# Kernel optimization log

Hardware: AMD Instinct MI355X
Metric: run time of the kernel (lower is better)

Reference implementation:

```python
import jax, jax.numpy as jnp
import numpy as np

# Hyperparameters (from init_kwargs)
N = 100000      # num_nodes
T = 4           # num_edge_type
E = 400000      # edges per type
C = 2           # num_channels
L = 2           # num_layers
W_IN = 128      # input feature dim
D = 64          # node_dim (w_out)
NUM_CLASS = 16
BETA = 0.5
M = 10000       # number of target nodes


def setup_inputs() -> dict:
    key = jax.random.key(0)
    ks = jax.random.split(key, 10)
    glorot = np.sqrt(6.0 / (W_IN + D))
    glorot1 = np.sqrt(6.0 / (C * D + D))
    glorot2 = np.sqrt(6.0 / (D + NUM_CLASS))
    return {
        "X": jax.random.normal(ks[0], (N, W_IN), dtype=jnp.float32),
        "edge_value": jax.random.uniform(ks[1], (T, E), dtype=jnp.float32),
        "conv_weights": 0.1 * jax.random.normal(ks[2], (L, C, T), dtype=jnp.float32),
        "Ws": jax.random.uniform(ks[3], (C, W_IN, D), minval=-glorot, maxval=glorot, dtype=jnp.float32),
        "lin1_w": jax.random.uniform(ks[4], (C * D, D), minval=-glorot1, maxval=glorot1, dtype=jnp.float32),
        "lin1_b": jnp.zeros((D,), dtype=jnp.float32),
        "lin_w": jax.random.uniform(ks[5], (D, NUM_CLASS), minval=-glorot2, maxval=glorot2, dtype=jnp.float32),
        "lin_b": jnp.zeros((NUM_CLASS,), dtype=jnp.float32),
        "edge_index": jax.random.randint(ks[6], (T, 2, E), 0, N),
        "target_x": jax.random.randint(ks[7], (M,), 0, N),
    }


def reference(X, edge_value, conv_weights, Ws, lin1_w, lin1_b, lin_w, lin_b,
              edge_index, target_x):
    # Flatten edge types into one big edge list. torch_sparse.coalesce(op='add')
    # followed by torch.sparse.mm is mathematically a duplicate-summing SpMM,
    # i.e. a segment_sum over destination rows.
    rows = edge_index[:, 0, :].reshape(-1)      # [T*E]
    cols = edge_index[:, 1, :].reshape(-1)      # [T*E]
    vals = edge_value.reshape(-1)               # [T*E]
    type_id = jnp.repeat(jnp.arange(T), E)      # [T*E] edge-type id (constant)

    # Per-channel input projections: X_ = X @ Ws[c]  -> [C, N, D]
    X_ = jnp.einsum('nf,cfd->cnd', X, Ws)
    H = X_

    for l in range(L):
        # FastGTConv: softmax over edge types per channel
        filt = jax.nn.softmax(conv_weights[l], axis=1)   # [C, T]
        newH = []
        for c in range(C):
            v = vals * filt[c, type_id]                  # [T*E] mixed edge weights
            msgs = v[:, None] * H[c][cols]               # gather + scale: [T*E, D]
            newH.append(jax.ops.segment_sum(msgs, rows, num_segments=N))
        H = jnp.stack(newH)                              # [C, N, D]

    # FastGTN tail: relu(beta*X_ + (1-beta)*H), concat channels, linear1
    Hc = jax.nn.relu(BETA * X_ + (1.0 - BETA) * H)       # [C, N, D]
    Hcat = jnp.transpose(Hc, (1, 0, 2)).reshape(N, C * D)
    H_ = Hcat @ lin1_w + lin1_b                          # [N, D]

    # FastGTNs head: logits at target nodes
    return H_[target_x] @ lin_w + lin_b                  # [M, NUM_CLASS]
```

## Files before the change

kernel.cpp:

```cpp
#include <hip/hip_runtime.h>

#define N_NODES   100000
#define T_TYPES   4
#define E_EDGES   400000
#define E4        100000
#define G_TOT     400000
#define TE_TOT    1600000
#define C_CH      2
#define L_LAYERS  2
#define W_INF     128
#define DD        64
#define NUM_CLASS 16
#define BETA      0.5f
#define M_TGT     10000

#define NBKT      196
#define BROWS     512
#define BPAD      9216
#define CHUNK_G   512
#define NPART_BLK ((G_TOT + CHUNK_G - 1) / CHUNK_G)

static const size_t PLANE2 = (size_t)N_NODES * DD;

typedef __attribute__((ext_vector_type(8))) short short8x;
typedef __attribute__((ext_vector_type(4))) float f32x4;

__device__ __forceinline__ unsigned bf16rne(float x) {
    unsigned u = __float_as_uint(x);
    return (u + 0x7FFFu + ((u >> 16) & 1u)) >> 16;
}
__device__ __forceinline__ unsigned packbf(float a, float b) {
    return bf16rne(a) | (bf16rne(b) << 16);
}
__device__ __forceinline__ float bflo(unsigned u) { return __uint_as_float(u << 16); }
__device__ __forceinline__ float bfhi(unsigned u) { return __uint_as_float(u & 0xFFFF0000u); }

__device__ __forceinline__ void load_filter(const float* cw, int layer,
                                            float* f0, float* f1) {
    float m0 = -1e30f, m1 = -1e30f;
    #pragma unroll
    for (int t = 0; t < T_TYPES; ++t) {
        f0[t] = cw[layer * C_CH * T_TYPES + t];
        f1[t] = cw[layer * C_CH * T_TYPES + T_TYPES + t];
        m0 = fmaxf(m0, f0[t]); m1 = fmaxf(m1, f1[t]);
    }
    float s0 = 0.f, s1 = 0.f;
    #pragma unroll
    for (int t = 0; t < T_TYPES; ++t) {
        f0[t] = __expf(f0[t] - m0); s0 += f0[t];
        f1[t] = __expf(f1[t] - m1); s1 += f1[t];
    }
    #pragma unroll
    for (int t = 0; t < T_TYPES; ++t) { f0[t] /= s0; f1[t] /= s1; }
}

__global__ void prep_kernel(const float* __restrict__ Ws,
                            unsigned short* __restrict__ Wsb,
                            int* __restrict__ cursor) {
    int b = blockIdx.x;
    int tid = threadIdx.x;
    if (b < 64) {
        int idx = b * 256 + tid;
        int c   = idx >> 13;
        int rem = idx & 8191;
        int d   = rem >> 7;
        int k   = rem & 127;
        Wsb[idx] = (unsigned short)bf16rne(Ws[c * (W_INF * DD) + k * DD + d]);
    } else {
        if (tid < NBKT) cursor[tid] = tid * BPAD;
    }
}

#define AROW 136
__global__ __launch_bounds__(256) void proj_mfma(const float* __restrict__ X,
                                                 const unsigned short* __restrict__ Wsb,
                                                 unsigned* __restrict__ Xp16) {
    __shared__ unsigned short a_lds[64 * AROW];
    int tid  = threadIdx.x;
    int row0 = blockIdx.x * 64;

    const float4* X4 = (const float4*)X;
    #pragma unroll
    for (int i = 0; i < 8; ++i) {
        int gi = tid + 256 * i;
        int r  = gi >> 5;
        int c4 = gi & 31;
        int row = row0 + r;
        float4 v = make_float4(0.f, 0.f, 0.f, 0.f);
        if (row < N_NODES) v = X4[(size_t)row * 32 + c4];
        *(uint2*)&a_lds[r * AROW + c4 * 4] = make_uint2(packbf(v.x, v.y),
                                                        packbf(v.z, v.w));
    }
    __syncthreads();

    int wave = tid >> 6, lane = tid & 63;
    int m = lane & 15, q = lane >> 4;

    short8x A[4];
    #pragma unroll
    for (int ks = 0; ks < 4; ++ks)
        A[ks] = *(const short8x*)&a_lds[(wave * 16 + m) * AROW + ks * 32 + q * 8];

    #pragma unroll
    for (int ct = 0; ct < 4; ++ct) {
        f32x4 acc0 = {0.f, 0.f, 0.f, 0.f};
        f32x4 acc1 = {0.f, 0.f, 0.f, 0.f};
        #pragma unroll
        for (int ks = 0; ks < 4; ++ks) {
            short8x B0 = *(const short8x*)(Wsb + (ct * 16 + m) * 128 + ks * 32 + q * 8);
            short8x B1 = *(const short8x*)(Wsb + 8192 + (ct * 16 + m) * 128 + ks * 32 + q * 8);
            acc0 = __builtin_amdgcn_mfma_f32_16x16x32_bf16(A[ks], B0, acc0, 0, 0, 0);
            acc1 = __builtin_amdgcn_mfma_f32_16x16x32_bf16(A[ks], B1, acc1, 0, 0, 0);
        }
        #pragma unroll
        for (int r = 0; r < 4; ++r) {
            int row = row0 + wave * 16 + q * 4 + r;
            if (row < N_NODES)
                Xp16[(size_t)row * DD + ct * 16 + m] = packbf(acc0[r], acc1[r]);
        }
    }
}

__global__ __launch_bounds__(256) void partition_kernel(const int* __restrict__ edge_index,
                                                        const float* __restrict__ edge_value,
                                                        const float* __restrict__ cw,
                                                        int* __restrict__ cursor,
                                                        int2* __restrict__ edata2) {
    __shared__ int cnt[NBKT];
    __shared__ int lbase[NBKT];
    __shared__ int gbase[NBKT];
    __shared__ int2 le[CHUNK_G * 4];
    __shared__ unsigned char lbk[CHUNK_G * 4];
    int tid = threadIdx.x;
    if (tid < NBKT) cnt[tid] = 0;
    __syncthreads();

    float f0[T_TYPES], f1[T_TYPES];
    load_filter(cw, 0, f0, f1);

    int px[8], pv[8], rk[8], bk[8];
    int ne = 0;
    #pragma unroll
    for (int g = 0; g < 2; ++g) {
        int idx = blockIdx.x * CHUNK_G + g * 256 + tid;
        if (idx < G_TOT) {
            int t = idx / E4, r = idx - t * E4;
            const int* bptr = edge_index + (size_t)t * 2 * E_EDGES;
            int4   rw = ((const int4*)bptr)[r];
            int4   cl = ((const int4*)(bptr + E_EDGES))[r];
            float4 vv = ((const float4*)(edge_value + (size_t)t * E_EDGES))[r];
            int tb = t << 17;
            int   rr[4] = {rw.x, rw.y, rw.z, rw.w};
            int   cc[4] = {cl.x, cl.y, cl.z, cl.w};
            float vf[4] = {vv.x, vv.y, vv.z, vv.w};
            #pragma unroll
            for (int k = 0; k < 4; ++k) {
                int b = rr[k] >> 9;
                px[ne] = cc[k] | tb | ((rr[k] & 511) << 19);
                pv[ne] = __float_as_int(vf[k]);
                bk[ne] = b;
                rk[ne] = atomicAdd(&cnt[b], 1);
                ++ne;
            }
        }
    }
    __syncthreads();
    if (tid < 64) {
        int c[4]; int s = 0;
        #pragma unroll
        for (int k = 0; k < 4; ++k) {
            int idx = tid * 4 + k;
            c[k] = (idx < NBKT) ? cnt[idx] : 0;
            s += c[k];
        }
        int inc = s;
        #pragma unroll
        for (int off = 1; off < 64; off <<= 1) {
            int v = __shfl_up(inc, off);
            if (tid >= off) inc += v;
        }
        int base = inc - s;
        #pragma unroll
        for (int k = 0; k < 4; ++k) {
            int idx = tid * 4 + k;
            if (idx < NBKT) lbase[idx] = base;
            base += c[k];
        }
    }
    __syncthreads();
    #pragma unroll
    for (int k = 0; k < 8; ++k) {
        if (k < ne) {
            int slot = lbase[bk[k]] + rk[k];
            le[slot]  = make_int2(px[k], pv[k]);
            lbk[slot] = (unsigned char)bk[k];
        }
    }
    __syncthreads();
    if (tid < NBKT) gbase[tid] = cnt[tid] ? atomicAdd(&cursor[tid], cnt[tid]) : 0;
    __syncthreads();
    int ngrp = min(CHUNK_G, G_TOT - blockIdx.x * CHUNK_G);
    int nloc = 4 * ngrp;
    for (int j = tid; j < nloc; j += 256) {
        int b = lbk[j];
        int2 e = le[j];
        int t = (e.x >> 17) & 3;
        float v = __int_as_float(e.y);
        edata2[gbase[b] + (j - lbase[b])] =
            make_int2(e.x, (int)packbf(v * f0[t], v * f1[t]));
    }
}

__global__ __launch_bounds__(1024) void rowsort_kernel(const int* __restrict__ cursor,
                                                       int2* __restrict__ edata2,
                                                       int* __restrict__ offs) {
    __shared__ int rcnt[BROWS];
    __shared__ int rbase[BROWS];
    __shared__ int rcur[BROWS];
    __shared__ int2 le[BPAD];
    int b   = blockIdx.x;
    int tid = threadIdx.x;
    int bb  = b * BPAD;
    int cnt = cursor[b] - bb;
    if (tid < BROWS) rcnt[tid] = 0;
    __syncthreads();
    for (int j = tid; j < cnt; j += 1024) {
        int2 e = edata2[bb + j];
        le[j] = e;
        atomicAdd(&rcnt[(e.x >> 19) & 511], 1);
    }
    __syncthreads();
    if (tid < 64) {
        int c[8]; int s = 0;
        #pragma unroll
        for (int k = 0; k < 8; ++k) { c[k] = rcnt[tid * 8 + k]; s += c[k]; }
        int inc = s;
        #pragma unroll
        for (int off = 1; off < 64; off <<= 1) {
            int v = __shfl_up(inc, off);
            if (tid >= off) inc += v;
        }
        int base = inc - s;
        #pragma unroll
        for (int k = 0; k < 8; ++k) { rbase[tid * 8 + k] = base; base += c[k]; }
    }
    __syncthreads();
    if (tid < BROWS) rcur[tid] = rbase[tid];
    __syncthreads();
    for (int j = tid; j < cnt; j += 1024) {
        int2 e = le[j];
        int lr = (e.x >> 19) & 511;
        int pos = atomicAdd(&rcur[lr], 1);
        edata2[bb + pos] = e;
    }
    int row0  = b * BROWS;
    int nrows = min(BROWS, N_NODES - row0);
    if (tid < nrows)
        offs[row0 + tid] = bb + rbase[tid] + rcnt[tid];
}

__device__ __forceinline__ void edge_fma(const uint2 h, unsigned wp, float4& acc) {
    float w0 = bflo(wp), w1 = bfhi(wp);
    acc.x = fmaf(w0, bflo(h.x), acc.x);
    acc.y = fmaf(w1, bfhi(h.x), acc.y);
    acc.z = fmaf(w0, bflo(h.y), acc.z);
    acc.w = fmaf(w1, bfhi(h.y), acc.w);
}

__device__ __forceinline__ int row_beg(const int* offs, int row) {
    return ((row & 511) == 0) ? (row >> 9) * BPAD : offs[row - 1];
}

__global__ __launch_bounds__(256) void spmm_gather(const uint2* __restrict__ Hin16,
                                                   uint2* __restrict__ Hout16,
                                                   const int* __restrict__ offs,
                                                   const int2* __restrict__ edata2) {
    int lane = threadIdx.x & 63;
    int slot = lane & 31, sub = lane >> 5;
    int row  = (blockIdx.x * blockDim.x + threadIdx.x) >> 6;
    int beg = row_beg(offs, row);
    int end = offs[row];
    float4 acc = make_float4(0.f, 0.f, 0.f, 0.f);
    int i = beg + sub;
    for (; i + 6 < end; i += 8) {
        int2 e0 = edata2[i];
        int2 e1 = edata2[i + 2];
        int2 e2 = edata2[i + 4];
        int2 e3 = edata2[i + 6];
        uint2 h0 = Hin16[(size_t)((e0.x & 0x1FFFF) * 32 + slot)];
        uint2 h1 = Hin16[(size_t)((e1.x & 0x1FFFF) * 32 + slot)];
        uint2 h2 = Hin16[(size_t)((e2.x & 0x1FFFF) * 32 + slot)];
        uint2 h3 = Hin16[(size_t)((e3.x & 0x1FFFF) * 32 + slot)];
        edge_fma(h0, (unsigned)e0.y, acc);
        edge_fma(h1, (unsigned)e1.y, acc);
        edge_fma(h2, (unsigned)e2.y, acc);
        edge_fma(h3, (unsigned)e3.y, acc);
    }
    for (; i < end; i += 2) {
        int2 e = edata2[i];
        uint2 h = Hin16[(size_t)((e.x & 0x1FFFF) * 32 + slot)];
        edge_fma(h, (unsigned)e.y, acc);
    }
    acc.x += __shfl_xor(acc.x, 32);
    acc.y += __shfl_xor(acc.y, 32);
    acc.z += __shfl_xor(acc.z, 32);
    acc.w += __shfl_xor(acc.w, 32);
    if (sub == 0)
        Hout16[(size_t)row * 32 + slot] = make_uint2(packbf(acc.x, acc.y),
                                                     packbf(acc.z, acc.w));
}

__global__ __launch_bounds__(256) void tgt_tail_kernel(const uint2* __restrict__ Hin16,
                                                       const unsigned* __restrict__ Xp16,
                                                       const int* __restrict__ offs,
                                                       const int2* __restrict__ edata2,
                                                       const float* __restrict__ cw,
                                                       const int* __restrict__ tgt,
                                                       const float* __restrict__ lin1_w,
                                                       const float* __restrict__ lin1_b,
                                                       const float* __restrict__ lin_w,
                                                       const float* __restrict__ lin_b,
                                                       float* __restrict__ out) {
    __shared__ float l1w[W_INF * DD];
    __shared__ float lw[DD * NUM_CLASS];
    __shared__ float l1b[DD];
    __shared__ float lb[NUM_CLASS];
    __shared__ float hc[4][W_INF];
    __shared__ float hmid[4][DD];

    int tid = threadIdx.x;
    {
        const float4* g = (const float4*)lin1_w;
        float4* s = (float4*)l1w;
        #pragma unroll
        for (int i = 0; i < 8; ++i) s[tid + 256 * i] = g[tid + 256 * i];
        ((float4*)lw)[tid] = ((const float4*)lin_w)[tid];
        if (tid < DD) l1b[tid] = lin1_b[tid];
        else if (tid < DD + NUM_CLASS) lb[tid - DD] = lin_b[tid - DD];
    }

    float f0a[T_TYPES], f1a[T_TYPES], f0b[T_TYPES], f1b[T_TYPES];
    load_filter(cw, 0, f0a, f1a);
    load_filter(cw, 1, f0b, f1b);
    float r0[T_TYPES], r1[T_TYPES];
    #pragma unroll
    for (int t = 0; t < T_TYPES; ++t) { r0[t] = f0b[t] / f0a[t]; r1[t] = f1b[t] / f1a[t]; }

    int w = tid >> 6, lane = tid & 63;
    int slot = lane & 31, sub = lane >> 5;
    int m = blockIdx.x * 4 + w;
    int row = tgt[m];
    int beg = row_beg(offs, row);
    int end = offs[row];
    float4 acc = make_float4(0.f, 0.f, 0.f, 0.f);
    for (int i = beg + sub; i < end; i += 2) {
        int2 e = edata2[i];
        int t = (e.x >> 17) & 3;
        uint2 h = Hin16[(size_t)((e.x & 0x1FFFF) * 32 + slot)];
        unsigned wp = (unsigned)e.y;
        float w0 = bflo(wp) * r0[t], w1 = bfhi(wp) * r1[t];
        acc.x = fmaf(w0, bflo(h.x), acc.x);
        acc.y = fmaf(w1, bfhi(h.x), acc.y);
        acc.z = fmaf(w0, bflo(h.y), acc.z);
        acc.w = fmaf(w1, bfhi(h.y), acc.w);
    }
    acc.x += __shfl_xor(acc.x, 32);
    acc.y += __shfl_xor(acc.y, 32);
    acc.z += __shfl_xor(acc.z, 32);
    acc.w += __shfl_xor(acc.w, 32);

    if (sub == 0) {
        uint2 xu = ((const uint2*)Xp16)[(size_t)row * 32 + slot];
        int d0 = 2 * slot, d1 = 2 * slot + 1;
        hc[w][d0]      = fmaxf(BETA * bflo(xu.x) + (1.f - BETA) * acc.x, 0.f);
        hc[w][DD + d0] = fmaxf(BETA * bfhi(xu.x) + (1.f - BETA) * acc.y, 0.f);
        hc[w][d1]      = fmaxf(BETA * bflo(xu.y) + (1.f - BETA) * acc.z, 0.f);
        hc[w][DD + d1] = fmaxf(BETA * bfhi(xu.y) + (1.f - BETA) * acc.w, 0.f);
    }
    __syncthreads();

    float a1 = l1b[lane];
    #pragma unroll 8
    for (int k = 0; k < W_INF; ++k)
        a1 = fmaf(hc[w][k], l1w[k * DD + lane], a1);
    hmid[w][lane] = a1;
    __syncthreads();

    if (lane < NUM_CLASS) {
        float o = lb[lane];
        #pragma unroll 8
        for (int k = 0; k < DD; ++k)
            o = fmaf(hmid[w][k], lw[k * NUM_CLASS + lane], o);
        out[(size_t)m * NUM_CLASS + lane] = o;
    }
}

extern "C" void kernel_launch(void* const* d_in, const int* in_sizes, int n_in,
                              void* d_out, int out_size, void* d_ws, size_t ws_size,
                              hipStream_t stream) {
    const float* X            = (const float*)d_in[0];
    const float* edge_value   = (const float*)d_in[1];
    const float* conv_weights = (const float*)d_in[2];
    const float* Ws           = (const float*)d_in[3];
    const float* lin1_w       = (const float*)d_in[4];
    const float* lin1_b       = (const float*)d_in[5];
    const float* lin_w        = (const float*)d_in[6];
    const float* lin_b        = (const float*)d_in[7];
    const int*   edge_index   = (const int*)d_in[8];
    const int*   target_x     = (const int*)d_in[9];
    float* out = (float*)d_out;

    unsigned*       Xp16 = (unsigned*)d_ws;
    unsigned*       H116 = Xp16 + PLANE2;
    unsigned short* Wsb  = (unsigned short*)(H116 + PLANE2);
    int*            offs = (int*)(Wsb + C_CH * W_INF * DD);
    int*            cursor = offs + N_NODES;
    int2*           edata2 = (int2*)(cursor + 256);

    prep_kernel<<<65, 256, 0, stream>>>(Ws, Wsb, cursor);
    partition_kernel<<<NPART_BLK, 256, 0, stream>>>(edge_index, edge_value,
                                                    conv_weights, cursor, edata2);
    proj_mfma<<<(N_NODES + 63) / 64, 256, 0, stream>>>(X, Wsb, Xp16);
    rowsort_kernel<<<NBKT, 1024, 0, stream>>>(cursor, edata2, offs);
    spmm_gather<<<(N_NODES * 64) / 256, 256, 0, stream>>>((const uint2*)Xp16,
                                                          (uint2*)H116, offs, edata2);
    tgt_tail_kernel<<<M_TGT / 4, 256, 0, stream>>>((const uint2*)H116, Xp16, offs,
                                                   edata2, conv_weights, target_x,
                                                   lin1_w, lin1_b, lin_w, lin_b, out);
}
```

Before: 273.5 us.

## Fuse partition with projection, shrink row buckets, widen gather loads to 16 bytes

Merges the edge-partition and MFMA projection kernels into one launch, with blocks picking their role from the block index, so the two independent phases can run together. Bucket size drops from 512 to 256 rows: more buckets, smaller padding, and a rowsort with 512 threads. The SpMM gather and target tail now load 16-byte uint4 chunks, with four edges in flight per wave and a two-step shuffle reduction. The risks are more shared memory per block in the fused kernel and less memory-level parallelism per lane in the gather.

```diff
diff --git a/kernel.cpp b/kernel.cpp
--- a/kernel.cpp
+++ b/kernel.cpp
@@ -14,11 +14,12 @@
 #define BETA      0.5f
 #define M_TGT     10000
 
-#define NBKT      196
-#define BROWS     512
-#define BPAD      9216
-#define CHUNK_G   512
-#define NPART_BLK ((G_TOT + CHUNK_G - 1) / CHUNK_G)
+#define NBKT      391
+#define BROWS     256
+#define BPAD      4864
+#define CHUNK_G   1024
+#define NPART_BLK 391
+#define PROJ_BLK  1563
 
 static const size_t PLANE2 = (size_t)N_NODES * DD;
 
@@ -67,153 +68,162 @@
         int k   = rem & 127;
         Wsb[idx] = (unsigned short)bf16rne(Ws[c * (W_INF * DD) + k * DD + d]);
     } else {
-        if (tid < NBKT) cursor[tid] = tid * BPAD;
+        int idx = (b - 64) * 256 + tid;
+        if (idx < NBKT) cursor[idx] = idx * BPAD;
     }
 }
 
 #define AROW 136
-__global__ __launch_bounds__(256) void proj_mfma(const float* __restrict__ X,
-                                                 const unsigned short* __restrict__ Wsb,
-                                                 unsigned* __restrict__ Xp16) {
-    __shared__ unsigned short a_lds[64 * AROW];
-    int tid  = threadIdx.x;
-    int row0 = blockIdx.x * 64;
-
-    const float4* X4 = (const float4*)X;
-    #pragma unroll
-    for (int i = 0; i < 8; ++i) {
-        int gi = tid + 256 * i;
-        int r  = gi >> 5;
-        int c4 = gi & 31;
-        int row = row0 + r;
-        float4 v = make_float4(0.f, 0.f, 0.f, 0.f);
-        if (row < N_NODES) v = X4[(size_t)row * 32 + c4];
-        *(uint2*)&a_lds[r * AROW + c4 * 4] = make_uint2(packbf(v.x, v.y),
-                                                        packbf(v.z, v.w));
-    }
-    __syncthreads();
-
-    int wave = tid >> 6, lane = tid & 63;
-    int m = lane & 15, q = lane >> 4;
-
-    short8x A[4];
-    #pragma unroll
-    for (int ks = 0; ks < 4; ++ks)
-        A[ks] = *(const short8x*)&a_lds[(wave * 16 + m) * AROW + ks * 32 + q * 8];
-
-    #pragma unroll
-    for (int ct = 0; ct < 4; ++ct) {
-        f32x4 acc0 = {0.f, 0.f, 0.f, 0.f};
-        f32x4 acc1 = {0.f, 0.f, 0.f, 0.f};
-        #pragma unroll
-        for (int ks = 0; ks < 4; ++ks) {
-            short8x B0 = *(const short8x*)(Wsb + (ct * 16 + m) * 128 + ks * 32 + q * 8);
-            short8x B1 = *(const short8x*)(Wsb + 8192 + (ct * 16 + m) * 128 + ks * 32 + q * 8);
-            acc0 = __builtin_amdgcn_mfma_f32_16x16x32_bf16(A[ks], B0, acc0, 0, 0, 0);
-            acc1 = __builtin_amdgcn_mfma_f32_16x16x32_bf16(A[ks], B1, acc1, 0, 0, 0);
-        }
-        #pragma unroll
-        for (int r = 0; r < 4; ++r) {
-            int row = row0 + wave * 16 + q * 4 + r;
-            if (row < N_NODES)
-                Xp16[(size_t)row * DD + ct * 16 + m] = packbf(acc0[r], acc1[r]);
-        }
-    }
-}
-
-__global__ __launch_bounds__(256) void partition_kernel(const int* __restrict__ edge_index,
-                                                        const float* __restrict__ edge_value,
-                                                        const float* __restrict__ cw,
-                                                        int* __restrict__ cursor,
-                                                        int2* __restrict__ edata2) {
-    __shared__ int cnt[NBKT];
-    __shared__ int lbase[NBKT];
-    __shared__ int gbase[NBKT];
-    __shared__ int2 le[CHUNK_G * 4];
-    __shared__ unsigned char lbk[CHUNK_G * 4];
+#define SMEM_BYTES 45664
+
+__global__ __launch_bounds__(256) void build_proj_kernel(
+        const int* __restrict__ edge_index,
+        const float* __restrict__ edge_value,
+        const float* __restrict__ cw,
+        int* __restrict__ cursor,
+        int2* __restrict__ edata2,
+        const float* __restrict__ X,
+        const unsigned short* __restrict__ Wsb,
+        unsigned* __restrict__ Xp16) {
+    __shared__ __align__(16) char smem[SMEM_BYTES];
     int tid = threadIdx.x;
-    if (tid < NBKT) cnt[tid] = 0;
-    __syncthreads();
-
-    float f0[T_TYPES], f1[T_TYPES];
-    load_filter(cw, 0, f0, f1);
-
-    int px[8], pv[8], rk[8], bk[8];
-    int ne = 0;
-    #pragma unroll
-    for (int g = 0; g < 2; ++g) {
-        int idx = blockIdx.x * CHUNK_G + g * 256 + tid;
-        if (idx < G_TOT) {
-            int t = idx / E4, r = idx - t * E4;
-            const int* bptr = edge_index + (size_t)t * 2 * E_EDGES;
-            int4   rw = ((const int4*)bptr)[r];
-            int4   cl = ((const int4*)(bptr + E_EDGES))[r];
-            float4 vv = ((const float4*)(edge_value + (size_t)t * E_EDGES))[r];
-            int tb = t << 17;
-            int   rr[4] = {rw.x, rw.y, rw.z, rw.w};
-            int   cc[4] = {cl.x, cl.y, cl.z, cl.w};
-            float vf[4] = {vv.x, vv.y, vv.z, vv.w};
+
+    if (blockIdx.x < NPART_BLK) {
+        int* cnt   = (int*)smem;
+        int* lbase = cnt + 392;
+        int* gbase = lbase + 392;
+        int2* le   = (int2*)(smem + 4704);
+        unsigned short* lbk = (unsigned short*)(smem + 4704 + 32768);
+
+        int p = blockIdx.x;
+        for (int j = tid; j < NBKT; j += 256) cnt[j] = 0;
+        __syncthreads();
+
+        float f0[T_TYPES], f1[T_TYPES];
+        load_filter(cw, 0, f0, f1);
+
+        int px[16], pv[16], rk[16], bk[16];
+        int ne = 0;
+        #pragma unroll
+        for (int g = 0; g < 4; ++g) {
+            int idx = p * CHUNK_G + g * 256 + tid;
+            if (idx < G_TOT) {
+                int t = idx / E4, r = idx - t * E4;
+                const int* bptr = edge_index + (size_t)t * 2 * E_EDGES;
+                int4   rw = ((const int4*)bptr)[r];
+                int4   cl = ((const int4*)(bptr + E_EDGES))[r];
+                float4 vv = ((const float4*)(edge_value + (size_t)t * E_EDGES))[r];
+                int tb = t << 17;
+                int   rr[4] = {rw.x, rw.y, rw.z, rw.w};
+                int   cc[4] = {cl.x, cl.y, cl.z, cl.w};
+                float vf[4] = {vv.x, vv.y, vv.z, vv.w};
+                #pragma unroll
+                for (int k = 0; k < 4; ++k) {
+                    int b = rr[k] >> 8;
+                    px[ne] = cc[k] | tb | ((rr[k] & 255) << 19);
+                    pv[ne] = __float_as_int(vf[k]);
+                    bk[ne] = b;
+                    rk[ne] = atomicAdd(&cnt[b], 1);
+                    ++ne;
+                }
+            }
+        }
+        __syncthreads();
+        if (tid < 64) {
+            int c[7]; int s = 0;
             #pragma unroll
-            for (int k = 0; k < 4; ++k) {
-                int b = rr[k] >> 9;
-                px[ne] = cc[k] | tb | ((rr[k] & 511) << 19);
-                pv[ne] = __float_as_int(vf[k]);
-                bk[ne] = b;
-                rk[ne] = atomicAdd(&cnt[b], 1);
-                ++ne;
-            }
-        }
-    }
-    __syncthreads();
-    if (tid < 64) {
-        int c[4]; int s = 0;
-        #pragma unroll
-        for (int k = 0; k < 4; ++k) {
-            int idx = tid * 4 + k;
-            c[k] = (idx < NBKT) ? cnt[idx] : 0;
-            s += c[k];
-        }
-        int inc = s;
-        #pragma unroll
-        for (int off = 1; off < 64; off <<= 1) {
-            int v = __shfl_up(inc, off);
-            if (tid >= off) inc += v;
-        }
-        int base = inc - s;
-        #pragma unroll
-        for (int k = 0; k < 4; ++k) {
-            int idx = tid * 4 + k;
-            if (idx < NBKT) lbase[idx] = base;
-            base += c[k];
-        }
-    }
-    __syncthreads();
-    #pragma unroll
-    for (int k = 0; k < 8; ++k) {
-        if (k < ne) {
-            int slot = lbase[bk[k]] + rk[k];
-            le[slot]  = make_int2(px[k], pv[k]);
-            lbk[slot] = (unsigned char)bk[k];
-        }
-    }
-    __syncthreads();
-    if (tid < NBKT) gbase[tid] = cnt[tid] ? atomicAdd(&cursor[tid], cnt[tid]) : 0;
-    __syncthreads();
-    int ngrp = min(CHUNK_G, G_TOT - blockIdx.x * CHUNK_G);
-    int nloc = 4 * ngrp;
-    for (int j = tid; j < nloc; j += 256) {
-        int b = lbk[j];
-        int2 e = le[j];
-        int t = (e.x >> 17) & 3;
-        float v = __int_as_float(e.y);
-        edata2[gbase[b] + (j - lbase[b])] =
-            make_int2(e.x, (int)packbf(v * f0[t], v * f1[t]));
-    }
-}
-
-__global__ __launch_bounds__(1024) void rowsort_kernel(const int* __restrict__ cursor,
-                                                       int2* __restrict__ edata2,
-                                                       int* __restrict__ offs) {
+            for (int k = 0; k < 7; ++k) {
+                int idx = tid * 7 + k;
+                c[k] = (idx < NBKT) ? cnt[idx] : 0;
+                s += c[k];
+            }
+            int inc = s;
+            #pragma unroll
+            for (int off = 1; off < 64; off <<= 1) {
+                int v = __shfl_up(inc, off);
+                if (tid >= off) inc += v;
+            }
+            int base = inc - s;
+            #pragma unroll
+            for (int k = 0; k < 7; ++k) {
+                int idx = tid * 7 + k;
+                if (idx < NBKT) lbase[idx] = base;
+                base += c[k];
+            }
+        }
+        __syncthreads();
+        #pragma unroll
+        for (int k = 0; k < 16; ++k) {
+            if (k < ne) {
+                int slot = lbase[bk[k]] + rk[k];
+                le[slot]  = make_int2(px[k], pv[k]);
+                lbk[slot] = (unsigned short)bk[k];
+            }
+        }
+        __syncthreads();
+        for (int j = tid; j < NBKT; j += 256)
+            gbase[j] = cnt[j] ? atomicAdd(&cursor[j], cnt[j]) : 0;
+        __syncthreads();
+        int ngrp = min(CHUNK_G, G_TOT - p * CHUNK_G);
+        int nloc = 4 * ngrp;
+        for (int j = tid; j < nloc; j += 256) {
+            int b = lbk[j];
+            int2 e = le[j];
+            int t = (e.x >> 17) & 3;
+            float v = __int_as_float(e.y);
+            edata2[gbase[b] + (j - lbase[b])] =
+                make_int2(e.x, (int)packbf(v * f0[t], v * f1[t]));
+        }
+    } else {
+        unsigned short* a_lds = (unsigned short*)smem;
+        int row0 = (blockIdx.x - NPART_BLK) * 64;
+
+        const float4* X4 = (const float4*)X;
+        #pragma unroll
+        for (int i = 0; i < 8; ++i) {
+            int gi = tid + 256 * i;
+            int r  = gi >> 5;
+            int c4 = gi & 31;
+            int row = row0 + r;
+            float4 v = make_float4(0.f, 0.f, 0.f, 0.f);
+            if (row < N_NODES) v = X4[(size_t)row * 32 + c4];
+            *(uint2*)&a_lds[r * AROW + c4 * 4] = make_uint2(packbf(v.x, v.y),
+                                                            packbf(v.z, v.w));
+        }
+        __syncthreads();
+
+        int wave = tid >> 6, lane = tid & 63;
+        int m = lane & 15, q = lane >> 4;
+
+        short8x A[4];
+        #pragma unroll
+        for (int ks = 0; ks < 4; ++ks)
+            A[ks] = *(const short8x*)&a_lds[(wave * 16 + m) * AROW + ks * 32 + q * 8];
+
+        #pragma unroll
+        for (int ct = 0; ct < 4; ++ct) {
+            f32x4 acc0 = {0.f, 0.f, 0.f, 0.f};
+            f32x4 acc1 = {0.f, 0.f, 0.f, 0.f};
+            #pragma unroll
+            for (int ks = 0; ks < 4; ++ks) {
+                short8x B0 = *(const short8x*)(Wsb + (ct * 16 + m) * 128 + ks * 32 + q * 8);
+                short8x B1 = *(const short8x*)(Wsb + 8192 + (ct * 16 + m) * 128 + ks * 32 + q * 8);
+                acc0 = __builtin_amdgcn_mfma_f32_16x16x32_bf16(A[ks], B0, acc0, 0, 0, 0);
+                acc1 = __builtin_amdgcn_mfma_f32_16x16x32_bf16(A[ks], B1, acc1, 0, 0, 0);
+            }
+            #pragma unroll
+            for (int r = 0; r < 4; ++r) {
+                int row = row0 + wave * 16 + q * 4 + r;
+                if (row < N_NODES)
+                    Xp16[(size_t)row * DD + ct * 16 + m] = packbf(acc0[r], acc1[r]);
+            }
+        }
+    }
+}
+
+__global__ __launch_bounds__(512) void rowsort_kernel(const int* __restrict__ cursor,
+                                                      int2* __restrict__ edata2,
+                                                      int* __restrict__ offs) {
     __shared__ int rcnt[BROWS];
     __shared__ int rbase[BROWS];
     __shared__ int rcur[BROWS];
@@ -224,16 +234,16 @@
     int cnt = cursor[b] - bb;
     if (tid < BROWS) rcnt[tid] = 0;
     __syncthreads();
-    for (int j = tid; j < cnt; j += 1024) {
+    for (int j = tid; j < cnt; j += 512) {
         int2 e = edata2[bb + j];
         le[j] = e;
-        atomicAdd(&rcnt[(e.x >> 19) & 511], 1);
+        atomicAdd(&rcnt[(e.x >> 19) & 255], 1);
     }
     __syncthreads();
     if (tid < 64) {
-        int c[8]; int s = 0;
-        #pragma unroll
-        for (int k = 0; k < 8; ++k) { c[k] = rcnt[tid * 8 + k]; s += c[k]; }
+        int c[4]; int s = 0;
+        #pragma unroll
+        for (int k = 0; k < 4; ++k) { c[k] = rcnt[tid * 4 + k]; s += c[k]; }
         int inc = s;
         #pragma unroll
         for (int off = 1; off < 64; off <<= 1) {
@@ -242,14 +252,14 @@
         }
         int base = inc - s;
         #pragma unroll
-        for (int k = 0; k < 8; ++k) { rbase[tid * 8 + k] = base; base += c[k]; }
+        for (int k = 0; k < 4; ++k) { rbase[tid * 4 + k] = base; base += c[k]; }
     }
     __syncthreads();
     if (tid < BROWS) rcur[tid] = rbase[tid];
     __syncthreads();
-    for (int j = tid; j < cnt; j += 1024) {
+    for (int j = tid; j < cnt; j += 512) {
         int2 e = le[j];
-        int lr = (e.x >> 19) & 511;
+        int lr = (e.x >> 19) & 255;
         int pos = atomicAdd(&rcur[lr], 1);
         edata2[bb + pos] = e;
     }
@@ -259,58 +269,68 @@
         offs[row0 + tid] = bb + rbase[tid] + rcnt[tid];
 }
 
-__device__ __forceinline__ void edge_fma(const uint2 h, unsigned wp, float4& acc) {
+__device__ __forceinline__ void qfma(const uint4 h, unsigned wp,
+                                     float4& a, float4& b) {
     float w0 = bflo(wp), w1 = bfhi(wp);
-    acc.x = fmaf(w0, bflo(h.x), acc.x);
-    acc.y = fmaf(w1, bfhi(h.x), acc.y);
-    acc.z = fmaf(w0, bflo(h.y), acc.z);
-    acc.w = fmaf(w1, bfhi(h.y), acc.w);
+    a.x = fmaf(w0, bflo(h.x), a.x);
+    a.y = fmaf(w1, bfhi(h.x), a.y);
+    a.z = fmaf(w0, bflo(h.y), a.z);
+    a.w = fmaf(w1, bfhi(h.y), a.w);
+    b.x = fmaf(w0, bflo(h.z), b.x);
+    b.y = fmaf(w1, bfhi(h.z), b.y);
+    b.z = fmaf(w0, bflo(h.w), b.z);
+    b.w = fmaf(w1, bfhi(h.w), b.w);
+}
+
+__device__ __forceinline__ void qreduce(float4& a, float4& b) {
+    a.x += __shfl_xor(a.x, 16); a.y += __shfl_xor(a.y, 16);
+    a.z += __shfl_xor(a.z, 16); a.w += __shfl_xor(a.w, 16);
+    b.x += __shfl_xor(b.x, 16); b.y += __shfl_xor(b.y, 16);
+    b.z += __shfl_xor(b.z, 16); b.w += __shfl_xor(b.w, 16);
+    a.x += __shfl_xor(a.x, 32); a.y += __shfl_xor(a.y, 32);
+    a.z += __shfl_xor(a.z, 32); a.w += __shfl_xor(a.w, 32);
+    b.x += __shfl_xor(b.x, 32); b.y += __shfl_xor(b.y, 32);
+    b.z += __shfl_xor(b.z, 32); b.w += __shfl_xor(b.w, 32);
 }
 
 __device__ __forceinline__ int row_beg(const int* offs, int row) {
-    return ((row & 511) == 0) ? (row >> 9) * BPAD : offs[row - 1];
-}
-
-__global__ __launch_bounds__(256) void spmm_gather(const uint2* __restrict__ Hin16,
-                                                   uint2* __restrict__ Hout16,
+    return ((row & 255) == 0) ? (row >> 8) * BPAD : offs[row - 1];
+}
+
+__global__ __launch_bounds__(256) void spmm_gather(const unsigned* __restrict__ Hin16,
+                                                   unsigned* __restrict__ Hout16,
                                                    const int* __restrict__ offs,
                                                    const int2* __restrict__ edata2) {
     int lane = threadIdx.x & 63;
-    int slot = lane & 31, sub = lane >> 5;
+    int s16 = lane & 15, sub = lane >> 4;
     int row  = (blockIdx.x * blockDim.x + threadIdx.x) >> 6;
     int beg = row_beg(offs, row);
     int end = offs[row];
-    float4 acc = make_float4(0.f, 0.f, 0.f, 0.f);
+    const uint4* hp = (const uint4*)Hin16;
+    float4 a = make_float4(0.f, 0.f, 0.f, 0.f);
+    float4 b = make_float4(0.f, 0.f, 0.f, 0.f);
     int i = beg + sub;
-    for (; i + 6 < end; i += 8) {
+    for (; i + 4 < end; i += 8) {
         int2 e0 = edata2[i];
-        int2 e1 = edata2[i + 2];
-        int2 e2 = edata2[i + 4];
-        int2 e3 = edata2[i + 6];
-        uint2 h0 = Hin16[(size_t)((e0.x & 0x1FFFF) * 32 + slot)];
-        uint2 h1 = Hin16[(size_t)((e1.x & 0x1FFFF) * 32 + slot)];
-        uint2 h2 = Hin16[(size_t)((e2.x & 0x1FFFF) * 32 + slot)];
-        uint2 h3 = Hin16[(size_t)((e3.x & 0x1FFFF) * 32 + slot)];
-        edge_fma(h0, (unsigned)e0.y, acc);
-        edge_fma(h1, (unsigned)e1.y, acc);
-        edge_fma(h2, (unsigned)e2.y, acc);
-        edge_fma(h3, (unsigned)e3.y, acc);
-    }
-    for (; i < end; i += 2) {
+        int2 e1 = edata2[i + 4];
+        uint4 h0 = hp[(size_t)(e0.x & 0x1FFFF) * 16 + s16];
+        uint4 h1 = hp[(size_t)(e1.x & 0x1FFFF) * 16 + s16];
+        qfma(h0, (unsigned)e0.y, a, b);
+        qfma(h1, (unsigned)e1.y, a, b);
+    }
+    if (i < end) {
         int2 e = edata2[i];
-        uint2 h = Hin16[(size_t)((e.x & 0x1FFFF) * 32 + slot)];
-        edge_fma(h, (unsigned)e.y, acc);
-    }
-    acc.x += __shfl_xor(acc.x, 32);
-    acc.y += __shfl_xor(acc.y, 32);
-    acc.z += __shfl_xor(acc.z, 32);
-    acc.w += __shfl_xor(acc.w, 32);
+        uint4 h = hp[(size_t)(e.x & 0x1FFFF) * 16 + s16];
+        qfma(h, (unsigned)e.y, a, b);
+    }
+    qreduce(a, b);
     if (sub == 0)
-        Hout16[(size_t)row * 32 + slot] = make_uint2(packbf(acc.x, acc.y),
-                                                     packbf(acc.z, acc.w));
-}
-
-__global__ __launch_bounds__(256) void tgt_tail_kernel(const uint2* __restrict__ Hin16,
+        ((uint4*)Hout16)[(size_t)row * 16 + s16] =
+            make_uint4(packbf(a.x, a.y), packbf(a.z, a.w),
+                       packbf(b.x, b.y), packbf(b.z, b.w));
+}
+
+__global__ __launch_bounds__(256) void tgt_tail_kernel(const unsigned* __restrict__ Hin16,
                                                        const unsigned* __restrict__ Xp16,
                                                        const int* __restrict__ offs,
                                                        const int2* __restrict__ edata2,
@@ -347,35 +367,42 @@
     for (int t = 0; t < T_TYPES; ++t) { r0[t] = f0b[t] / f0a[t]; r1[t] = f1b[t] / f1a[t]; }
 
     int w = tid >> 6, lane = tid & 63;
-    int slot = lane & 31, sub = lane >> 5;
+    int s16 = lane & 15, sub = lane >> 4;
     int m = blockIdx.x * 4 + w;
     int row = tgt[m];
     int beg = row_beg(offs, row);
     int end = offs[row];
-    float4 acc = make_float4(0.f, 0.f, 0.f, 0.f);
-    for (int i = beg + sub; i < end; i += 2) {
+    const uint4* hp = (const uint4*)Hin16;
+    float4 a = make_float4(0.f, 0.f, 0.f, 0.f);
+    float4 b = make_float4(0.f, 0.f, 0.f, 0.f);
+    for (int i = beg + sub; i < end; i += 4) {
         int2 e = edata2[i];
         int t = (e.x >> 17) & 3;
-        uint2 h = Hin16[(size_t)((e.x & 0x1FFFF) * 32 + slot)];
+        uint4 h = hp[(size_t)(e.x & 0x1FFFF) * 16 + s16];
         unsigned wp = (unsigned)e.y;
         float w0 = bflo(wp) * r0[t], w1 = bfhi(wp) * r1[t];
-        acc.x = fmaf(w0, bflo(h.x), acc.x);
-        acc.y = fmaf(w1, bfhi(h.x), acc.y);
-        acc.z = fmaf(w0, bflo(h.y), acc.z);
-        acc.w = fmaf(w1, bfhi(h.y), acc.w);
-    }
-    acc.x += __shfl_xor(acc.x, 32);
-    acc.y += __shfl_xor(acc.y, 32);
-    acc.z += __shfl_xor(acc.z, 32);
-    acc.w += __shfl_xor(acc.w, 32);
+        a.x = fmaf(w0, bflo(h.x), a.x);
+        a.y = fmaf(w1, bfhi(h.x), a.y);
+        a.z = fmaf(w0, bflo(h.y), a.z);
+        a.w = fmaf(w1, bfhi(h.y), a.w);
+        b.x = fmaf(w0, bflo(h.z), b.x);
+        b.y = fmaf(w1, bfhi(h.z), b.y);
+        b.z = fmaf(w0, bflo(h.w), b.z);
+        b.w = fmaf(w1, bfhi(h.w), b.w);
+    }
+    qreduce(a, b);
 
     if (sub == 0) {
-        uint2 xu = ((const uint2*)Xp16)[(size_t)row * 32 + slot];
-        int d0 = 2 * slot, d1 = 2 * slot + 1;
-        hc[w][d0]      = fmaxf(BETA * bflo(xu.x) + (1.f - BETA) * acc.x, 0.f);
-        hc[w][DD + d0] = fmaxf(BETA * bfhi(xu.x) + (1.f - BETA) * acc.y, 0.f);
-        hc[w][d1]      = fmaxf(BETA * bflo(xu.y) + (1.f - BETA) * acc.z, 0.f);
-        hc[w][DD + d1] = fmaxf(BETA * bfhi(xu.y) + (1.f - BETA) * acc.w, 0.f);
+        uint4 xu = ((const uint4*)Xp16)[(size_t)row * 16 + s16];
+        int d0 = 4 * s16;
+        hc[w][d0 + 0]      = fmaxf(BETA * bflo(xu.x) + (1.f - BETA) * a.x, 0.f);
+        hc[w][DD + d0 + 0] = fmaxf(BETA * bfhi(xu.x) + (1.f - BETA) * a.y, 0.f);
+        hc[w][d0 + 1]      = fmaxf(BETA * bflo(xu.y) + (1.f - BETA) * a.z, 0.f);
+        hc[w][DD + d0 + 1] = fmaxf(BETA * bfhi(xu.y) + (1.f - BETA) * a.w, 0.f);
+        hc[w][d0 + 2]      = fmaxf(BETA * bflo(xu.z) + (1.f - BETA) * b.x, 0.f);
+        hc[w][DD + d0 + 2] = fmaxf(BETA * bfhi(xu.z) + (1.f - BETA) * b.y, 0.f);
+        hc[w][d0 + 3]      = fmaxf(BETA * bflo(xu.w) + (1.f - BETA) * b.z, 0.f);
+        hc[w][DD + d0 + 3] = fmaxf(BETA * bfhi(xu.w) + (1.f - BETA) * b.w, 0.f);
     }
     __syncthreads();
 
@@ -415,16 +442,14 @@
     unsigned short* Wsb  = (unsigned short*)(H116 + PLANE2);
     int*            offs = (int*)(Wsb + C_CH * W_INF * DD);
     int*            cursor = offs + N_NODES;
-    int2*           edata2 = (int2*)(cursor + 256);
-
-    prep_kernel<<<65, 256, 0, stream>>>(Ws, Wsb, cursor);
-    partition_kernel<<<NPART_BLK, 256, 0, stream>>>(edge_index, edge_value,
-                                                    conv_weights, cursor, edata2);
-    proj_mfma<<<(N_NODES + 63) / 64, 256, 0, stream>>>(X, Wsb, Xp16);
-    rowsort_kernel<<<NBKT, 1024, 0, stream>>>(cursor, edata2, offs);
-    spmm_gather<<<(N_NODES * 64) / 256, 256, 0, stream>>>((const uint2*)Xp16,
-                                                          (uint2*)H116, offs, edata2);
-    tgt_tail_kernel<<<M_TGT / 4, 256, 0, stream>>>((const uint2*)H116, Xp16, offs,
-                                                   edata2, conv_weights, target_x,
+    int2*           edata2 = (int2*)(cursor + 512);
+
+    prep_kernel<<<66, 256, 0, stream>>>(Ws, Wsb, cursor);
+    build_proj_kernel<<<NPART_BLK + PROJ_BLK, 256, 0, stream>>>(
+        edge_index, edge_value, conv_weights, cursor, edata2, X, Wsb, Xp16);
+    rowsort_kernel<<<NBKT, 512, 0, stream>>>(cursor, edata2, offs);
+    spmm_gather<<<(N_NODES * 64) / 256, 256, 0, stream>>>(Xp16, H116, offs, edata2);
+    tgt_tail_kernel<<<M_TGT / 4, 256, 0, stream>>>(H116, Xp16, offs, edata2,
+                                                   conv_weights, target_x,
                                                    lin1_w, lin1_b, lin_w, lin_b, out);
 }
```

Measured after the change: 253.0 us. 1.08x faster.
